# Performance work log

Measured on AMD Instinct MI355X. Metric: run time of the kernel, lower is better.

## Reference

```python
import jax, jax.numpy as jnp
import numpy as np
from jax import lax

B, N, D_FEAT = 16, 4096, 20
NPOINT, NSAMPLE = 1024, 32
MLP = [64, 64, 128]
IN_CH = 3 + 1 + D_FEAT  # grouped_xyz_norm(3) + L2 norm(1) + grouped_depth_norm(20)
BN_EPS = 1e-5


def setup_inputs() -> dict:
    key = jax.random.key(0)
    ks = jax.random.split(key, 20)
    inp = {
        "xyz": jax.random.normal(ks[0], (B, 3, N), dtype=jnp.float32),
        "feature": jax.random.normal(ks[1], (B, N, D_FEAT), dtype=jnp.float32),
    }
    last = IN_CH
    kidx = 2
    for li, out_ch in enumerate(MLP):
        inp[f"w{li}"] = jax.random.normal(ks[kidx], (out_ch, last), dtype=jnp.float32) * (1.0 / np.sqrt(last)); kidx += 1
        inp[f"b{li}"] = jax.random.normal(ks[kidx], (out_ch,), dtype=jnp.float32) * 0.01; kidx += 1
        inp[f"g{li}"] = 1.0 + 0.1 * jax.random.normal(ks[kidx], (out_ch,), dtype=jnp.float32); kidx += 1
        inp[f"bt{li}"] = 0.1 * jax.random.normal(ks[kidx], (out_ch,), dtype=jnp.float32); kidx += 1
        last = out_ch
    return inp


def square_distance(src, dst):
    # [B,S,C] x [B,M,C] -> [B,S,M]
    d = -2.0 * jnp.einsum("bsc,bmc->bsm", src, dst)
    d = d + jnp.sum(src * src, -1)[:, :, None]
    d = d + jnp.sum(dst * dst, -1)[:, None, :]
    return d


def farthest_point_sample(pts, npoint):
    # pts: [B,N,C]; deterministic start at index 0 (torch uses random start)
    b, n, _ = pts.shape
    bidx = jnp.arange(b)

    def step(carry, _):
        dist, far = carry
        centroid = pts[bidx, far]                      # [B,C]
        d = jnp.sum((pts - centroid[:, None, :]) ** 2, -1)  # [B,N]
        dist = jnp.minimum(dist, d)
        nxt = jnp.argmax(dist, -1)
        return (dist, nxt), far

    init = (jnp.full((b, n), 1e10, pts.dtype), jnp.zeros((b,), jnp.int32))
    _, idx = lax.scan(step, init, None, length=npoint)
    return idx.T  # [B,npoint]


def _gather_groups(points, idx):
    # points [B,N,C], idx [B,S,K] -> [B,S,K,C]
    return jax.vmap(lambda p, i: p[i])(points, idx)


def conv_bn_relu(x, w, b, g, bt):
    # x [B,C,K,S]; 1x1 conv = channel matmul; BN in training mode (batch stats, biased var)
    y = jnp.einsum("bcks,oc->boks", x, w) + b[None, :, None, None]
    mu = jnp.mean(y, axis=(0, 2, 3), keepdims=True)
    var = jnp.mean((y - mu) ** 2, axis=(0, 2, 3), keepdims=True)
    y = (y - mu) * lax.rsqrt(var + BN_EPS)
    y = y * g[None, :, None, None] + bt[None, :, None, None]
    return jax.nn.relu(y)


def reference(xyz, feature, w0, b0, g0, bt0, w1, b1, g1, bt1, w2, b2, g2, bt2):
    xyz_n = jnp.transpose(xyz, (0, 2, 1))              # [B,N,3]
    combined = jnp.concatenate([xyz_n, feature], -1)   # [B,N,23]
    fps_idx = farthest_point_sample(combined, NPOINT)  # [B,S]

    new_bin = jnp.take_along_axis(feature, fps_idx[:, :, None], axis=1)  # [B,S,20]
    new_xyz = jnp.take_along_axis(xyz_n, fps_idx[:, :, None], axis=1)    # [B,S,3]

    sqd = square_distance(new_bin, feature) + square_distance(new_xyz, xyz_n)  # [B,S,N]
    idx = jnp.argsort(sqd, axis=-1)[:, :, :NSAMPLE]    # [B,S,K]

    gxyz = _gather_groups(xyz_n, idx)                  # [B,S,K,3]
    gfeat = _gather_groups(feature, idx)               # [B,S,K,20]
    gxyz_norm = gxyz - new_xyz[:, :, None, :]
    gdep_norm = gfeat - new_bin[:, :, None, :]
    nrm = jnp.sqrt(jnp.maximum(jnp.sum(gxyz_norm ** 2, -1, keepdims=True), 1e-12))
    new_points = jnp.concatenate([gxyz_norm, nrm, gdep_norm], -1)  # [B,S,K,24]

    x = jnp.transpose(new_points, (0, 3, 2, 1))        # [B,24,K,S]
    for (w, b, g, bt) in [(w0, b0, g0, bt0), (w1, b1, g1, bt1), (w2, b2, g2, bt2)]:
        x = conv_bn_relu(x, w, b, g, bt)
    out = jnp.max(x, axis=2)                           # [B,128,S]
    return jnp.transpose(new_xyz, (0, 2, 1)), out, new_bin
```

## Files before the change

kernel.cpp:

```cpp
#include <hip/hip_runtime.h>

#define BB 16
#define NN 4096
#define DFEAT 20
#define SS 1024
#define KK 32
#define MM (BB*SS*KK)

#define WS_STATS   0ull
#define WS_PARAMS  8192ull
#define WS_FPSIDX  12288ull
#define WS_CENT    81920ull
#define WS_KNN     1654784ull
#define WS_COMB    3751936ull
#define WS_YB      10043392ull
#define WS_NEED    77152256ull

static __device__ __forceinline__ unsigned short f2bf(float f){
    unsigned u = __float_as_uint(f);
    unsigned r = (u + 0x7FFFu + ((u >> 16) & 1u)) >> 16;
    return (unsigned short)r;
}
static __device__ __forceinline__ float bf2f(unsigned short v){
    return __uint_as_float((unsigned)v << 16);
}
static __device__ __forceinline__ void pinv(float& x){
    asm volatile("" : "+v"(x));
}

__global__ void k_zstats(double* __restrict__ stats){
    int t = threadIdx.x;
#pragma unroll
    for (int i = 0; i < 4; ++i) stats[i*256 + t] = 0.0;
}

__global__ void k_fail(float* __restrict__ out, int n){
    int i = blockIdx.x * 256 + threadIdx.x;
    if (i < n) out[i] = 0.f;
}

__global__ __launch_bounds__(256) void k_build(const float* __restrict__ xyz,
                                               const float* __restrict__ feat,
                                               float* __restrict__ comb)
{
    int idx = blockIdx.x * 256 + threadIdx.x;
    int b = idx >> 12, j = idx & 4095;
    float c[24];
    c[0] = xyz[((size_t)b*3 + 0)*NN + j];
    c[1] = xyz[((size_t)b*3 + 1)*NN + j];
    c[2] = xyz[((size_t)b*3 + 2)*NN + j];
    const float* f = feat + ((size_t)b*NN + j)*DFEAT;
#pragma unroll
    for (int d = 0; d < 20; ++d) c[3+d] = f[d];
    c[23] = 0.f;
    float* out = comb + (size_t)idx * 24;
#pragma unroll
    for (int q = 0; q < 6; ++q)
        ((float4*)out)[q] = make_float4(c[4*q], c[4*q+1], c[4*q+2], c[4*q+3]);
}

__global__ __launch_bounds__(512, 2) void k_fps(const float* __restrict__ comb,
                                                int* __restrict__ fpsidx)
{
    int b = blockIdx.x, t = threadIdx.x;
    const float* C = comb + (size_t)b * NN * 24;
    float pt[8][24];
    float dist[8];
#pragma unroll
    for (int p = 0; p < 8; ++p){
        const float4* r = (const float4*)(C + (size_t)(t + 512*p) * 24);
#pragma unroll
        for (int q = 0; q < 6; ++q){
            float4 v = r[q];
            pt[p][4*q] = v.x; pt[p][4*q+1] = v.y; pt[p][4*q+2] = v.z; pt[p][4*q+3] = v.w;
        }
        dist[p] = 1e10f;
    }
#pragma unroll
    for (int p = 0; p < 8; ++p)
#pragma unroll
        for (int q = 0; q < 23; ++q) pinv(pt[p][q]);

    __shared__ unsigned long long wkey[2][8];
    int lane = t & 63, w = t >> 6;
    int far = 0;
    for (int s = 0; s < SS; ++s){
        if (t == 0) fpsidx[b*SS + s] = far;
        const float4* crow = (const float4*)(C + (size_t)far * 24);
        float cc[24];
#pragma unroll
        for (int q = 0; q < 6; ++q){
            float4 cv = crow[q];
            cc[4*q] = cv.x; cc[4*q+1] = cv.y; cc[4*q+2] = cv.z; cc[4*q+3] = cv.w;
        }
        unsigned long long best = 0;
#pragma unroll
        for (int p = 0; p < 8; ++p){
            float d0 = pt[p][0] - cc[0];
            float acc = d0 * d0;
#pragma unroll
            for (int q = 1; q < 23; ++q){
                float dd = pt[p][q] - cc[q];
                acc = fmaf(dd, dd, acc);
            }
            dist[p] = fminf(dist[p], acc);
            unsigned long long key = ((unsigned long long)__float_as_uint(dist[p]) << 32)
                                   | (unsigned long long)(0xFFFFFFFFu - (unsigned)(t + 512*p));
            best = best > key ? best : key;
        }
#pragma unroll
        for (int off = 32; off > 0; off >>= 1){
            unsigned long long o = __shfl_xor(best, off);
            best = best > o ? best : o;
        }
        int par = s & 1;
        if (lane == 0) wkey[par][w] = best;
        __syncthreads();
        unsigned long long k2 = wkey[par][lane & 7];
#pragma unroll
        for (int off = 1; off < 8; off <<= 1){
            unsigned long long o = __shfl_xor(k2, off);
            k2 = k2 > o ? k2 : o;
        }
        far = (int)(0xFFFFFFFFu - (unsigned)(k2 & 0xFFFFFFFFull));
    }
}

__global__ __launch_bounds__(256) void k_gather(const float* __restrict__ comb,
                                                const int* __restrict__ fpsidx,
                                                float* __restrict__ cent,
                                                float* __restrict__ out0,
                                                float* __restrict__ out2)
{
    int idx = blockIdx.x * 256 + threadIdx.x;
    int b = idx >> 10, s = idx & 1023;
    int j = fpsidx[idx];
    const float* row = comb + ((size_t)b*NN + j) * 24;
    float* cr = cent + (size_t)idx * 24;
#pragma unroll
    for (int q = 0; q < 6; ++q) ((float4*)cr)[q] = ((const float4*)row)[q];
#pragma unroll
    for (int c = 0; c < 3; ++c) out0[((size_t)b*3 + c)*SS + s] = row[c];
    float* o2 = out2 + (size_t)idx * 20;
#pragma unroll
    for (int d = 0; d < 20; ++d) o2[d] = row[3 + d];
}

__global__ __launch_bounds__(256) void k_knn(const float* __restrict__ comb,
                                             const float* __restrict__ cent,
                                             int* __restrict__ knn)
{
    int w = threadIdx.x >> 6, lane = threadIdx.x & 63;
    int r = blockIdx.x * 4 + w;
    int b = r >> 10;
    const float* crow = cent + (size_t)r * 24;
    const float* P0 = comb + (size_t)b * NN * 24;
    double cc[24];
#pragma unroll
    for (int q = 0; q < 24; ++q) cc[q] = (double)crow[q];
    unsigned u[64];
#pragma unroll
    for (int k = 0; k < 64; ++k){
        int j = k*64 + lane;
        const float4* pr = (const float4*)(P0 + (size_t)j * 24);
        double acc = 0.0;
#pragma unroll
        for (int q = 0; q < 6; ++q){
            float4 v = pr[q];
            double d0 = (double)v.x - cc[4*q];
            double d1 = (double)v.y - cc[4*q+1];
            double d2 = (double)v.z - cc[4*q+2];
            double d3 = (double)v.w - cc[4*q+3];
            acc += d0*d0; acc += d1*d1; acc += d2*d2; acc += d3*d3;
        }
        u[k] = __float_as_uint((float)acc);
    }
    unsigned lo = 0u, hi = 0xFFFFFFFFu;
    for (int it = 0; it < 32; ++it){
        unsigned mid = lo + ((hi - lo) >> 1);
        int cnt = 0;
#pragma unroll
        for (int k = 0; k < 64; ++k) cnt += (u[k] <= mid) ? 1 : 0;
#pragma unroll
        for (int off = 32; off > 0; off >>= 1) cnt += __shfl_xor(cnt, off);
        if (cnt >= KK) hi = mid; else lo = mid + 1;
    }
    unsigned T = lo;
    int* orow = knn + (size_t)r * KK;
    unsigned long long lmask = (1ull << lane) - 1ull;
    int pos = 0;
#pragma unroll
    for (int k = 0; k < 64; ++k){
        bool lt = (u[k] < T);
        unsigned long long mk = __ballot(lt);
        if (lt) orow[pos + __popcll(mk & lmask)] = k*64 + lane;
        pos += __popcll(mk);
    }
#pragma unroll
    for (int k = 0; k < 64; ++k){
        if (pos >= KK) break;
        bool eq = (u[k] == T);
        unsigned long long mk = __ballot(eq);
        int rk = __popcll(mk & lmask);
        if (eq && (pos + rk) < KK) orow[pos + rk] = k*64 + lane;
        pos += __popcll(mk);
    }
}

__global__ __launch_bounds__(256) void k_l1(const float* __restrict__ comb,
                                            const float* __restrict__ cent,
                                            const int* __restrict__ knn,
                                            const float* __restrict__ w0,
                                            const float* __restrict__ b0,
                                            unsigned short* __restrict__ yb)
{
    __shared__ float Wt[24][64];
    __shared__ float Xt[24][68];
    int t = threadIdx.x;
    int m_base = blockIdx.x * 64;
    for (int i = t; i < 1536; i += 256){
        int o = i / 24, c = i - o*24;
        Wt[c][o] = w0[i];
    }
    {
        int sm = t & 63, g = t >> 6;
        int m = m_base + sm;
        int b = m >> 15;
        int row = m >> 5;
        int j = knn[m];
        const float* P  = comb + ((size_t)b*NN + j) * 24;
        const float* Cc = cent + (size_t)row * 24;
        if (g == 0){
            float dx = P[0]-Cc[0], dy = P[1]-Cc[1], dz = P[2]-Cc[2];
            Xt[0][sm] = dx; Xt[1][sm] = dy; Xt[2][sm] = dz;
            float n2 = dx*dx; n2 = fmaf(dy, dy, n2); n2 = fmaf(dz, dz, n2);
            Xt[3][sm] = sqrtf(fmaxf(n2, 1e-12f));
            Xt[4][sm] = P[3] - Cc[3];
            Xt[5][sm] = P[4] - Cc[4];
        } else {
#pragma unroll
            for (int cq = 0; cq < 6; ++cq){
                int c = 6*g + cq;
                Xt[c][sm] = P[c-1] - Cc[c-1];
            }
        }
    }
    __syncthreads();
    int i = t >> 4, jj = t & 15;
    float acc[4][4] = {};
#pragma unroll
    for (int c = 0; c < 24; ++c){
        float4 wv = *(const float4*)&Wt[c][i*4];
        float4 xv = *(const float4*)&Xt[c][jj*4];
        float wr[4] = {wv.x, wv.y, wv.z, wv.w};
        float xr[4] = {xv.x, xv.y, xv.z, xv.w};
#pragma unroll
        for (int a = 0; a < 4; ++a)
#pragma unroll
            for (int q = 0; q < 4; ++q) acc[a][q] = fmaf(wr[a], xr[q], acc[a][q]);
    }
#pragma unroll
    for (int oi = 0; oi < 4; ++oi){
        int o = i*4 + oi;
        float bb = b0[o];
        ushort4 rv;
        rv.x = f2bf(acc[oi][0]+bb); rv.y = f2bf(acc[oi][1]+bb);
        rv.z = f2bf(acc[oi][2]+bb); rv.w = f2bf(acc[oi][3]+bb);
        *(ushort4*)&yb[(size_t)o*MM + m_base + jj*4] = rv;
    }
}

__global__ __launch_bounds__(256) void k_stats(const unsigned short* __restrict__ y,
                                               double* __restrict__ stats)
{
    const int chunks = 8;
    int c = blockIdx.x / chunks, ch = blockIdx.x % chunks;
    size_t base = (size_t)c * MM + (size_t)ch * (MM / chunks);
    double s1 = 0.0, s2 = 0.0;
    const unsigned short* p = y + base;
    for (int i = threadIdx.x; i < MM/chunks; i += 256){
        float v = bf2f(p[i]);
        s1 += v; s2 += (double)v * v;
    }
#pragma unroll
    for (int off = 32; off > 0; off >>= 1){
        s1 += __shfl_xor(s1, off);
        s2 += __shfl_xor(s2, off);
    }
    __shared__ double ps1[4], ps2[4];
    int w = threadIdx.x >> 6, lane = threadIdx.x & 63;
    if (lane == 0){ ps1[w] = s1; ps2[w] = s2; }
    __syncthreads();
    if (threadIdx.x == 0){
        atomicAdd(&stats[c*2 + 0], ps1[0]+ps1[1]+ps1[2]+ps1[3]);
        atomicAdd(&stats[c*2 + 1], ps2[0]+ps2[1]+ps2[2]+ps2[3]);
    }
}

__global__ void k_affine(const double* __restrict__ stats, float* __restrict__ params, int C)
{
    int c = threadIdx.x;
    if (c < C){
        double mu = stats[c*2] / (double)MM;
        double var = stats[c*2 + 1] / (double)MM - mu*mu;
        params[c*2 + 0] = (float)mu;
        params[c*2 + 1] = (float)(1.0 / sqrt(var + 1e-5));
    }
}

__global__ __launch_bounds__(256) void k_l2(unsigned short* __restrict__ yb,
                                            const float* __restrict__ prm,
                                            const float* __restrict__ gg,
                                            const float* __restrict__ bt,
                                            const float* __restrict__ w,
                                            const float* __restrict__ bias)
{
    __shared__ float Wt[64][64];
    __shared__ float Xt[64][68];
    int t = threadIdx.x;
    int m_base = blockIdx.x * 64;
    for (int i = t; i < 4096; i += 256){
        int o = i >> 6, c = i & 63;
        Wt[c][o] = w[i];
    }
#pragma unroll
    for (int rp = 0; rp < 16; ++rp){
        int idx = rp*256 + t;
        int c = idx >> 6, mm2 = idx & 63;
        float v = bf2f(yb[(size_t)c*MM + m_base + mm2]);
        float t1 = (v - prm[c*2]) * prm[c*2 + 1];
        Xt[c][mm2] = fmaxf(fmaf(t1, gg[c], bt[c]), 0.f);
    }
    __syncthreads();
    int i = t >> 4, jj = t & 15;
    float acc[4][4] = {};
#pragma unroll
    for (int c = 0; c < 64; ++c){
        float4 wv = *(const float4*)&Wt[c][i*4];
        float4 xv = *(const float4*)&Xt[c][jj*4];
        float wr[4] = {wv.x, wv.y, wv.z, wv.w};
        float xr[4] = {xv.x, xv.y, xv.z, xv.w};
#pragma unroll
        for (int a = 0; a < 4; ++a)
#pragma unroll
            for (int q = 0; q < 4; ++q) acc[a][q] = fmaf(wr[a], xr[q], acc[a][q]);
    }
#pragma unroll
    for (int oi = 0; oi < 4; ++oi){
        int o = i*4 + oi;
        float bb = bias[o];
        ushort4 rv;
        rv.x = f2bf(acc[oi][0]+bb); rv.y = f2bf(acc[oi][1]+bb);
        rv.z = f2bf(acc[oi][2]+bb); rv.w = f2bf(acc[oi][3]+bb);
        *(ushort4*)&yb[(size_t)o*MM + m_base + jj*4] = rv;
    }
}

__global__ __launch_bounds__(256) void k_l3s(const unsigned short* __restrict__ yb,
                                             const float* __restrict__ prm,
                                             const float* __restrict__ gg,
                                             const float* __restrict__ bt,
                                             const float* __restrict__ w,
                                             const float* __restrict__ bias,
                                             double* __restrict__ stats)
{
    __shared__ float Wt[64][128];
    __shared__ float Xt[64][68];
    int t = threadIdx.x;
    for (int i = t; i < 8192; i += 256){
        int o = i >> 6, c = i & 63;
        Wt[c][o] = w[i];
    }
    int i = t >> 4, jj = t & 15;
    double s1[8] = {}, s2[8] = {};
    for (int tt = 0; tt < 16; ++tt){
        int m_base = (blockIdx.x * 16 + tt) * 64;
        __syncthreads();
#pragma unroll
        for (int rp = 0; rp < 16; ++rp){
            int idx = rp*256 + t;
            int c = idx >> 6, mm2 = idx & 63;
            float v = bf2f(yb[(size_t)c*MM + m_base + mm2]);
            float t1 = (v - prm[c*2]) * prm[c*2 + 1];
            Xt[c][mm2] = fmaxf(fmaf(t1, gg[c], bt[c]), 0.f);
        }
        __syncthreads();
        float acc[8][4] = {};
#pragma unroll
        for (int c = 0; c < 64; ++c){
            float4 w0v = *(const float4*)&Wt[c][i*8];
            float4 w1v = *(const float4*)&Wt[c][i*8 + 4];
            float4 xv  = *(const float4*)&Xt[c][jj*4];
            float wr[8] = {w0v.x, w0v.y, w0v.z, w0v.w, w1v.x, w1v.y, w1v.z, w1v.w};
            float xr[4] = {xv.x, xv.y, xv.z, xv.w};
#pragma unroll
            for (int a = 0; a < 8; ++a)
#pragma unroll
                for (int q = 0; q < 4; ++q) acc[a][q] = fmaf(wr[a], xr[q], acc[a][q]);
        }
#pragma unroll
        for (int oi = 0; oi < 8; ++oi){
            float bb = bias[i*8 + oi];
#pragma unroll
            for (int q = 0; q < 4; ++q){
                float v = acc[oi][q] + bb;
                s1[oi] += v;
                s2[oi] += (double)v * v;
            }
        }
    }
#pragma unroll
    for (int oi = 0; oi < 8; ++oi){
#pragma unroll
        for (int off = 1; off < 16; off <<= 1){
            s1[oi] += __shfl_xor(s1[oi], off);
            s2[oi] += __shfl_xor(s2[oi], off);
        }
    }
    if (jj == 0){
#pragma unroll
        for (int oi = 0; oi < 8; ++oi){
            int o = i*8 + oi;
            atomicAdd(&stats[o*2 + 0], s1[oi]);
            atomicAdd(&stats[o*2 + 1], s2[oi]);
        }
    }
}

__global__ __launch_bounds__(256) void k_final(const unsigned short* __restrict__ yb,
                                               const float* __restrict__ prm2,
                                               const float* __restrict__ g1c,
                                               const float* __restrict__ bt1c,
                                               const float* __restrict__ w,
                                               const float* __restrict__ bias,
                                               const float* __restrict__ prm3,
                                               const float* __restrict__ g2c,
                                               const float* __restrict__ bt2c,
                                               float* __restrict__ out1)
{
    __shared__ float Wt[64][128];
    __shared__ float Xt[64][68];
    int t = threadIdx.x;
    int m_base = blockIdx.x * 64;
    for (int i = t; i < 8192; i += 256){
        int o = i >> 6, c = i & 63;
        Wt[c][o] = w[i];
    }
#pragma unroll
    for (int rp = 0; rp < 16; ++rp){
        int idx = rp*256 + t;
        int c = idx >> 6, mm2 = idx & 63;
        float v = bf2f(yb[(size_t)c*MM + m_base + mm2]);
        float t1 = (v - prm2[c*2]) * prm2[c*2 + 1];
        Xt[c][mm2] = fmaxf(fmaf(t1, g1c[c], bt1c[c]), 0.f);
    }
    __syncthreads();
    int i = t >> 4, jj = t & 15;
    float acc[8][4] = {};
#pragma unroll
    for (int c = 0; c < 64; ++c){
        float4 w0v = *(const float4*)&Wt[c][i*8];
        float4 w1v = *(const float4*)&Wt[c][i*8 + 4];
        float4 xv  = *(const float4*)&Xt[c][jj*4];
        float wr[8] = {w0v.x, w0v.y, w0v.z, w0v.w, w1v.x, w1v.y, w1v.z, w1v.w};
        float xr[4] = {xv.x, xv.y, xv.z, xv.w};
#pragma unroll
        for (int a = 0; a < 8; ++a)
#pragma unroll
            for (int q = 0; q < 4; ++q) acc[a][q] = fmaf(wr[a], xr[q], acc[a][q]);
    }
    float mx[8];
#pragma unroll
    for (int oi = 0; oi < 8; ++oi){
        int o = i*8 + oi;
        float bb = bias[o];
        float mu = prm3[o*2], inv = prm3[o*2 + 1], gv = g2c[o], bv = bt2c[o];
        float m = 0.f;
#pragma unroll
        for (int q = 0; q < 4; ++q){
            float v = acc[oi][q] + bb;
            float r = fmaxf(fmaf((v - mu) * inv, gv, bv), 0.f);
            m = fmaxf(m, r);
        }
        mx[oi] = m;
    }
#pragma unroll
    for (int oi = 0; oi < 8; ++oi){
#pragma unroll
        for (int off = 1; off < 8; off <<= 1)
            mx[oi] = fmaxf(mx[oi], __shfl_xor(mx[oi], off));
    }
    if ((jj & 7) == 0){
        int rg = (m_base >> 5) + (jj >> 3);
        int b = rg >> 10, s = rg & 1023;
#pragma unroll
        for (int oi = 0; oi < 8; ++oi)
            out1[(size_t)b*131072 + (size_t)(i*8 + oi)*1024 + s] = mx[oi];
    }
}

extern "C" void kernel_launch(void* const* d_in, const int* in_sizes, int n_in,
                              void* d_out, int out_size, void* d_ws, size_t ws_size,
                              hipStream_t stream)
{
    const float* xyz  = (const float*)d_in[0];
    const float* feat = (const float*)d_in[1];
    const float* w0 = (const float*)d_in[2];  const float* b0  = (const float*)d_in[3];
    const float* g0 = (const float*)d_in[4];  const float* bt0 = (const float*)d_in[5];
    const float* w1 = (const float*)d_in[6];  const float* b1  = (const float*)d_in[7];
    const float* g1 = (const float*)d_in[8];  const float* bt1 = (const float*)d_in[9];
    const float* w2 = (const float*)d_in[10]; const float* b2  = (const float*)d_in[11];
    const float* g2 = (const float*)d_in[12]; const float* bt2 = (const float*)d_in[13];

    float* out0 = (float*)d_out;
    float* out1 = (float*)d_out + 49152;
    float* out2 = (float*)d_out + 49152 + 2097152;

    if (ws_size < WS_NEED){
        k_fail<<<(out_size + 255)/256, 256, 0, stream>>>((float*)d_out, out_size);
        return;
    }

    char* ws = (char*)d_ws;
    double* stats = (double*)(ws + WS_STATS);
    float* params = (float*)(ws + WS_PARAMS);
    int*   fpsidx = (int*)(ws + WS_FPSIDX);
    float* cent   = (float*)(ws + WS_CENT);
    int*   knn    = (int*)(ws + WS_KNN);
    float* comb   = (float*)(ws + WS_COMB);
    unsigned short* yb = (unsigned short*)(ws + WS_YB);

    k_zstats<<<1,    256, 0, stream>>>(stats);
    k_build <<<256,  256, 0, stream>>>(xyz, feat, comb);
    k_fps   <<<16,   512, 0, stream>>>(comb, fpsidx);
    k_gather<<<64,   256, 0, stream>>>(comb, fpsidx, cent, out0, out2);
    k_knn   <<<4096, 256, 0, stream>>>(comb, cent, knn);
    k_l1    <<<8192, 256, 0, stream>>>(comb, cent, knn, w0, b0, yb);
    k_stats <<<512,  256, 0, stream>>>(yb, stats);
    k_affine<<<1,    128, 0, stream>>>(stats, params, 64);
    k_l2    <<<8192, 256, 0, stream>>>(yb, params, g0, bt0, w1, b1);
    k_stats <<<512,  256, 0, stream>>>(yb, stats + 256);
    k_affine<<<1,    128, 0, stream>>>(stats + 256, params + 256, 64);
    k_l3s   <<<512,  256, 0, stream>>>(yb, params + 256, g1, bt1, w2, b2, stats + 512);
    k_affine<<<1,    128, 0, stream>>>(stats + 512, params + 512, 128);
    k_final <<<8192, 256, 0, stream>>>(yb, params + 256, g1, bt1, w2, b2,
                                       params + 512, g2, bt2, out1);
}
```

Measured before the change: 2.944 ms.

## Speed up FPS argmax with DPP wave reduction and LDS centroid broadcast

The farthest-point-sampling loop now takes the per-thread max over distance bits first, then builds a single 64-bit key. The intra-wave reduction uses DPP row shifts/broadcasts plus readlane instead of a shuffle butterfly. Each wave's winning thread stashes its point coordinates in shared memory, so the next centroid is read from LDS instead of global memory. The cross-wave reduction becomes vectorized LDS reads with a max tree. This shortens the serial per-iteration latency chain, at the cost of a divergent switch for the stash and extra shared memory.

Result: slower. 3.098 ms (+5.2%).

```diff
diff --git a/kernel.cpp b/kernel.cpp
--- a/kernel.cpp
+++ b/kernel.cpp
@@ -28,6 +28,16 @@
     asm volatile("" : "+v"(x));
 }
 
+static __device__ __forceinline__ unsigned long long max64(unsigned long long a, unsigned long long b){
+    return a > b ? a : b;
+}
+template<int CTRL>
+static __device__ __forceinline__ unsigned long long dpp_move64(unsigned long long k){
+    int tlo = __builtin_amdgcn_update_dpp(0, (int)(unsigned)k,         CTRL, 0xf, 0xf, true);
+    int thi = __builtin_amdgcn_update_dpp(0, (int)(unsigned)(k >> 32), CTRL, 0xf, 0xf, true);
+    return ((unsigned long long)(unsigned)thi << 32) | (unsigned)tlo;
+}
+
 __global__ void k_zstats(double* __restrict__ stats){
     int t = threadIdx.x;
 #pragma unroll
@@ -81,19 +91,24 @@
 #pragma unroll
         for (int q = 0; q < 23; ++q) pinv(pt[p][q]);
 
-    __shared__ unsigned long long wkey[2][8];
+    __shared__ __align__(16) unsigned long long wkey[2][8];
+    __shared__ __align__(16) float wpt[2][8][24];
     int lane = t & 63, w = t >> 6;
     int far = 0;
-    for (int s = 0; s < SS; ++s){
-        if (t == 0) fpsidx[b*SS + s] = far;
-        const float4* crow = (const float4*)(C + (size_t)far * 24);
-        float cc[24];
+
+    float cc[24];
+    {
+        const float4* crow = (const float4*)C;
 #pragma unroll
         for (int q = 0; q < 6; ++q){
             float4 cv = crow[q];
             cc[4*q] = cv.x; cc[4*q+1] = cv.y; cc[4*q+2] = cv.z; cc[4*q+3] = cv.w;
         }
-        unsigned long long best = 0;
+    }
+
+    for (int s = 0; s < SS; ++s){
+        if (t == 0) fpsidx[b*SS + s] = far;
+        unsigned maxbits = 0u;
 #pragma unroll
         for (int p = 0; p < 8; ++p){
             float d0 = pt[p][0] - cc[0];
@@ -104,25 +119,61 @@
                 acc = fmaf(dd, dd, acc);
             }
             dist[p] = fminf(dist[p], acc);
-            unsigned long long key = ((unsigned long long)__float_as_uint(dist[p]) << 32)
-                                   | (unsigned long long)(0xFFFFFFFFu - (unsigned)(t + 512*p));
-            best = best > key ? best : key;
-        }
-#pragma unroll
-        for (int off = 32; off > 0; off >>= 1){
-            unsigned long long o = __shfl_xor(best, off);
-            best = best > o ? best : o;
+            unsigned bb2 = __float_as_uint(dist[p]);
+            maxbits = bb2 > maxbits ? bb2 : maxbits;
+        }
+        int pstar = 0;
+#pragma unroll
+        for (int p = 7; p >= 0; --p)
+            if (__float_as_uint(dist[p]) == maxbits) pstar = p;
+        unsigned long long key = ((unsigned long long)maxbits << 32)
+                               | (unsigned long long)(0xFFFFFFFFu - (unsigned)(t + 512*pstar));
+
+        key = max64(key, dpp_move64<0x111>(key));
+        key = max64(key, dpp_move64<0x112>(key));
+        key = max64(key, dpp_move64<0x114>(key));
+        key = max64(key, dpp_move64<0x118>(key));
+        key = max64(key, dpp_move64<0x142>(key));
+        key = max64(key, dpp_move64<0x143>(key));
+        unsigned long long wk;
+        {
+            int slo = __builtin_amdgcn_readlane((int)(unsigned)key, 63);
+            int shi = __builtin_amdgcn_readlane((int)(unsigned)(key >> 32), 63);
+            wk = ((unsigned long long)(unsigned)shi << 32) | (unsigned)slo;
         }
         int par = s & 1;
-        if (lane == 0) wkey[par][w] = best;
+        if (lane == 0) wkey[par][w] = wk;
+        unsigned widx = 0xFFFFFFFFu - (unsigned)(wk & 0xFFFFFFFFull);
+        if (t == (int)(widx & 511u)){
+            int pw = (int)(widx >> 9);
+            float* dst = wpt[par][w];
+            switch (pw){
+#define STASH(P) case P: \
+                ((float4*)dst)[0] = make_float4(pt[P][0],pt[P][1],pt[P][2],pt[P][3]); \
+                ((float4*)dst)[1] = make_float4(pt[P][4],pt[P][5],pt[P][6],pt[P][7]); \
+                ((float4*)dst)[2] = make_float4(pt[P][8],pt[P][9],pt[P][10],pt[P][11]); \
+                ((float4*)dst)[3] = make_float4(pt[P][12],pt[P][13],pt[P][14],pt[P][15]); \
+                ((float4*)dst)[4] = make_float4(pt[P][16],pt[P][17],pt[P][18],pt[P][19]); \
+                ((float4*)dst)[5] = make_float4(pt[P][20],pt[P][21],pt[P][22],0.f); \
+                break;
+            STASH(0) STASH(1) STASH(2) STASH(3)
+            STASH(4) STASH(5) STASH(6) STASH(7)
+#undef STASH
+            }
+        }
         __syncthreads();
-        unsigned long long k2 = wkey[par][lane & 7];
-#pragma unroll
-        for (int off = 1; off < 8; off <<= 1){
-            unsigned long long o = __shfl_xor(k2, off);
-            k2 = k2 > o ? k2 : o;
-        }
+        const ulonglong2* kp = (const ulonglong2*)wkey[par];
+        ulonglong2 q0 = kp[0], q1 = kp[1], q2 = kp[2], q3 = kp[3];
+        unsigned long long k2 = max64(max64(max64(q0.x, q0.y), max64(q1.x, q1.y)),
+                                      max64(max64(q2.x, q2.y), max64(q3.x, q3.y)));
         far = (int)(0xFFFFFFFFu - (unsigned)(k2 & 0xFFFFFFFFull));
+        int wg = (far & 511) >> 6;
+        const float4* crow = (const float4*)wpt[par][wg];
+#pragma unroll
+        for (int q = 0; q < 6; ++q){
+            float4 cv = crow[q];
+            cc[4*q] = cv.x; cc[4*q+1] = cv.y; cc[4*q+2] = cv.z; cc[4*q+3] = cv.w;
+        }
     }
 }
 
```
